# Performance work log

Measured on AMD Instinct MI355X. Metric: run time of the kernel, lower is better.

## Reference

```python
import jax, jax.numpy as jnp
import numpy as np

L, B, H, R = 128, 4, 768, 97
LN_EPS = 1e-5


def setup_inputs() -> dict:
    key = jax.random.key(0)
    ks = jax.random.split(key, 8)
    s = 0.02
    return {
        "h_re1": jax.random.normal(ks[0], (L, B, H), jnp.float32),
        "h_re2": jax.random.normal(ks[1], (L, B, H), jnp.float32),
        "mask": jax.random.uniform(ks[2], (L, B), jnp.float32),
        "Wr": jax.random.normal(ks[3], (H, 2 * H), jnp.float32) * s,
        "br": jnp.zeros((H,), jnp.float32),
        "Wh": jax.random.normal(ks[4], (H, 3 * H), jnp.float32) * s,
        "bh": jnp.zeros((H,), jnp.float32),
        "gamma": jnp.ones((H,), jnp.float32),
        "beta": jnp.zeros((H,), jnp.float32),
        "Wo": jax.random.normal(ks[5], (R, H), jnp.float32) * s,
        "bo": jnp.zeros((R,), jnp.float32),
    }


def reference(h_re1, h_re2, mask, Wr, br, Wh, bh, gamma, beta, Wo, bo):
    # h_re1, h_re2: [L, B, H]; mask: [L, B]
    h = h_re2.shape[-1]
    # global context: tanh(Linear(cat(h_re1,h_re2))), max over length -> [B, H]
    g = jnp.tanh(jnp.einsum('lbi,hi->lbh', jnp.concatenate([h_re1, h_re2], axis=-1), Wr) + br)
    g = jnp.max(g, axis=0)  # [B, H]
    # hid2hid(cat(r1, r2, g)) == r1 @ W1.T + r2 @ W2.T + g @ W3.T + b
    # (avoids materializing the [L,L,B,3H] repeat+cat tensor)
    W1, W2, W3 = Wh[:, :h], Wh[:, h:2 * h], Wh[:, 2 * h:]
    a = jnp.einsum('lbi,hi->lbh', h_re2, W1)          # varies over first pair axis
    b2 = jnp.einsum('lbi,hi->lbh', h_re2, W2)         # varies over second pair axis
    gp = jnp.einsum('bi,hi->bh', g, W3) + bh          # constant over pairs
    pre = a[:, None, :, :] + b2[None, :, :, :] + gp   # [L, L, B, H]
    # LayerNorm over last dim (biased variance, as in torch)
    mu = jnp.mean(pre, axis=-1, keepdims=True)
    var = jnp.var(pre, axis=-1, keepdims=True)
    x = (pre - mu) * jax.lax.rsqrt(var + LN_EPS) * gamma + beta
    x = jax.nn.elu(x)  # dropout is identity in eval mode
    out = jax.nn.sigmoid(jnp.einsum('klbh,rh->klbr', x, Wo) + bo)  # [L, L, B, R]
    # pairwise mask: mask_e1 * mask_e2, broadcast over relation dim
    m = mask[:, None, :, None] * mask[None, :, :, None]
    return out * m
```

## Files before the change

kernel.cpp:

```cpp
#include <hip/hip_runtime.h>
#include <hip/hip_bf16.h>
#include <stdint.h>

#define L_ 128
#define B_ 4
#define H_ 768
#define R_ 97
#define LN_EPS 1e-5f

typedef _Float16 f16x8 __attribute__((ext_vector_type(8)));
typedef _Float16 f16x4 __attribute__((ext_vector_type(4)));
typedef _Float16 f16x2 __attribute__((ext_vector_type(2)));
typedef float f32x4 __attribute__((ext_vector_type(4)));

__global__ __launch_bounds__(256) void prep_all(const float* __restrict__ h1,
                                                const float* __restrict__ h2,
                                                const float* __restrict__ Wr,
                                                const float* __restrict__ Wh,
                                                const float* __restrict__ Wo,
                                                const float* __restrict__ gamma,
                                                const float* __restrict__ beta,
                                                _Float16* __restrict__ ccH,
                                                _Float16* __restrict__ Bp,
                                                _Float16* __restrict__ WoP,
                                                _Float16* __restrict__ gbH) {
  int blk = blockIdx.x;
  if (blk < 512) {
    const float2* s1 = (const float2*)(h1 + (size_t)blk * H_);
    const float2* s2 = (const float2*)(h2 + (size_t)blk * H_);
    f16x2* d = (f16x2*)(ccH + (size_t)blk * (2 * H_));
    for (int i = threadIdx.x; i < H_ / 2; i += 256) {
      float2 v = s1[i]; f16x2 o; o[0] = (_Float16)v.x; o[1] = (_Float16)v.y; d[i] = o;
    }
    for (int i = threadIdx.x; i < H_ / 2; i += 256) {
      float2 v = s2[i]; f16x2 o; o[0] = (_Float16)v.x; o[1] = (_Float16)v.y; d[H_ / 2 + i] = o;
    }
    return;
  }
  blk -= 512;
  if (blk < 6912) {
    int f = (blk * 256 + threadIdx.x) * 2;
    int j = f & 7;
    int u = f >> 3;
    int lidx = u & 63; u >>= 6;
    int nt = u % 144;
    int ks = u / 144;
    int k = ks * 32 + (lidx >> 4) * 8 + j;
    int n = nt * 16 + (lidx & 15);
    float v0, v1;
    if (n < 768) {
      v0 = Wr[(size_t)n * 1536 + k];
      v1 = Wr[(size_t)n * 1536 + k + 1];
    } else if (n < 1536) {
      int n2 = n - 768;
      if (k >= 768) { v0 = Wh[(size_t)n2 * 2304 + (k - 768)]; v1 = Wh[(size_t)n2 * 2304 + (k - 767)]; }
      else { v0 = 0.f; v1 = 0.f; }
    } else {
      int n2 = n - 1536;
      if (k >= 768) { v0 = Wh[(size_t)n2 * 2304 + 768 + (k - 768)]; v1 = Wh[(size_t)n2 * 2304 + 768 + (k - 767)]; }
      else { v0 = 0.f; v1 = 0.f; }
    }
    f16x2 o; o[0] = (_Float16)v0; o[1] = (_Float16)v1;
    *(f16x2*)(Bp + f) = o;
    return;
  }
  blk -= 6912;
  if (blk < 192) {
    int f = (blk * 256 + threadIdx.x) * 2;
    int j = f & 7;
    int u = f >> 3;
    int lidx = u & 63; u >>= 6;
    int nt = u & 7;
    int ks = u >> 3;
    int k = ks * 32 + (lidx >> 4) * 8 + j;
    int n = nt * 16 + (lidx & 15);
    float v0 = 0.f, v1 = 0.f;
    if (n < R_) { v0 = Wo[(size_t)n * H_ + k]; v1 = Wo[(size_t)n * H_ + k + 1]; }
    f16x2 o; o[0] = (_Float16)v0; o[1] = (_Float16)v1;
    *(f16x2*)(WoP + f) = o;
    return;
  }
  blk -= 192;
  int i = blk * 256 + threadIdx.x;
  if (i < H_) {
    gbH[i] = (_Float16)gamma[i];
    gbH[H_ + i] = (_Float16)beta[i];
  }
}

__global__ __launch_bounds__(256) void gemm_big(const _Float16* __restrict__ A,
                                                const _Float16* __restrict__ Bp,
                                                const float* __restrict__ br,
                                                unsigned int* __restrict__ gmaxU,
                                                _Float16* __restrict__ aH,
                                                _Float16* __restrict__ bH) {
  int w = threadIdx.x >> 6, l = threadIdx.x & 63;
  int nb = blockIdx.x, mb = blockIdx.y;
  int row0 = mb * 32 + (w & 1) * 16;
  int nt0 = nb * 4 + (w >> 1) * 2;
  const f16x8* ap = (const f16x8*)(A + (size_t)(row0 + (l & 15)) * 1536 + (l >> 4) * 8);
  const f16x8* bp = (const f16x8*)(Bp + ((size_t)nt0 * 64 + l) * 8);
  f32x4 acc0 = {}, acc1 = {};
  f16x8 ac = ap[0], b0c = bp[0], b1c = bp[64];
  for (int ks = 0; ks < 48; ++ks) {
    f16x8 an = {}, b0n = {}, b1n = {};
    if (ks < 47) {
      an = ap[(ks + 1) * 4];
      b0n = bp[(size_t)(ks + 1) * 9216];
      b1n = bp[(size_t)(ks + 1) * 9216 + 64];
    }
    acc0 = __builtin_amdgcn_mfma_f32_16x16x32_f16(ac, b0c, acc0, 0, 0, 0);
    acc1 = __builtin_amdgcn_mfma_f32_16x16x32_f16(ac, b1c, acc1, 0, 0, 0);
    ac = an; b0c = b0n; b1c = b1n;
  }
#pragma unroll
  for (int q = 0; q < 2; ++q) {
    f32x4 acc = q ? acc1 : acc0;
    int col = nb * 64 + (w >> 1) * 32 + q * 16 + (l & 15);
#pragma unroll
    for (int r = 0; r < 4; ++r) {
      int row = row0 + (l >> 4) * 4 + r;
      float v = acc[r];
      if (col < 768) {
        float t = tanhf(v + br[col]) + 1.0f;
        atomicMax(&gmaxU[(row & 3) * H_ + col], __float_as_uint(t));
      } else if (col < 1536) {
        aH[(size_t)row * H_ + (col - 768)] = (_Float16)v;
      } else {
        bH[(size_t)row * H_ + (col - 1536)] = (_Float16)v;
      }
    }
  }
}

__global__ __launch_bounds__(256) void gp_kernel(const float* __restrict__ Wh,
                                                 const unsigned int* __restrict__ gmaxU,
                                                 const float* __restrict__ bh,
                                                 float* __restrict__ gpv) {
  int n = blockIdx.x;
  int w = threadIdx.x >> 6, l = threadIdx.x & 63;
  const float* wr = Wh + (size_t)n * 2304 + 1536;
  const unsigned int* gm = gmaxU + (size_t)w * H_;
  float s = 0.f;
#pragma unroll
  for (int t = 0; t < 12; ++t) {
    int i = l + 64 * t;
    s += wr[i] * (__uint_as_float(gm[i]) - 1.0f);
  }
#pragma unroll
  for (int off = 32; off; off >>= 1) s += __shfl_xor(s, off);
  if (l == 0) gpv[(size_t)w * H_ + n] = s + bh[n];
}

__global__ __launch_bounds__(256) void stats(const _Float16* __restrict__ aH,
                                             const _Float16* __restrict__ bH,
                                             const float* __restrict__ gpv,
                                             _Float16* __restrict__ aH2,
                                             float* __restrict__ S,
                                             float* __restrict__ Q) {
  int r = blockIdx.x * 4 + (threadIdx.x >> 6);
  int l = threadIdx.x & 63;
  float s = 0.f, q = 0.f;
  if (r < 512) {
    int b = r & 3;
    const f16x4* ap = (const f16x4*)(aH + (size_t)r * H_);
    const float4* gp4 = (const float4*)(gpv + (size_t)b * H_);
    f16x4* op = (f16x4*)(aH2 + (size_t)r * H_);
#pragma unroll
    for (int t = 0; t < 3; ++t) {
      int i = t * 64 + l;
      f16x4 av = ap[i];
      float4 g4 = gp4[i];
      f16x4 o;
      o[0] = (_Float16)((float)av[0] + g4.x);
      o[1] = (_Float16)((float)av[1] + g4.y);
      o[2] = (_Float16)((float)av[2] + g4.z);
      o[3] = (_Float16)((float)av[3] + g4.w);
      op[i] = o;
#pragma unroll
      for (int j = 0; j < 4; ++j) { float y = (float)o[j]; s += y; q += y * y; }
    }
  } else {
    const f16x4* bp = (const f16x4*)(bH + (size_t)(r - 512) * H_);
#pragma unroll
    for (int t = 0; t < 3; ++t) {
      f16x4 bv = bp[t * 64 + l];
#pragma unroll
      for (int j = 0; j < 4; ++j) { float y = (float)bv[j]; s += y; q += y * y; }
    }
  }
#pragma unroll
  for (int off = 32; off; off >>= 1) {
    s += __shfl_xor(s, off);
    q += __shfl_xor(q, off);
  }
  if (l == 0) { S[r] = s; Q[r] = q; }
}

__global__ __launch_bounds__(256) void dotab(const _Float16* __restrict__ aH2,
                                             const _Float16* __restrict__ bH,
                                             const float* __restrict__ S,
                                             const float* __restrict__ Q,
                                             float* __restrict__ mu_arr,
                                             float* __restrict__ rs_arr) {
  int w = threadIdx.x >> 6, l = threadIdx.x & 63;
  int ltq = blockIdx.x, kt = blockIdx.y, b = blockIdx.z;
  int lt = ltq * 4 + w;
  const f16x8* ap = (const f16x8*)(aH2 + ((size_t)(kt * 16 + (l & 15)) * 4 + b) * H_ + (l >> 4) * 8);
  const f16x8* bp = (const f16x8*)(bH + ((size_t)(lt * 16 + (l & 15)) * 4 + b) * H_ + (l >> 4) * 8);
  f32x4 acc = {};
  f16x8 a0 = ap[0], b0 = bp[0], a1 = ap[4], b1 = bp[4];
  for (int ks = 0; ks < 24; ++ks) {
    f16x8 a2 = {}, b2 = {};
    if (ks < 22) { a2 = ap[(ks + 2) * 4]; b2 = bp[(ks + 2) * 4]; }
    acc = __builtin_amdgcn_mfma_f32_16x16x32_f16(a0, b0, acc, 0, 0, 0);
    a0 = a1; b0 = b1; a1 = a2; b1 = b2;
  }
#pragma unroll
  for (int r = 0; r < 4; ++r) {
    int k = kt * 16 + (l >> 4) * 4 + r;
    int lg = lt * 16 + (l & 15);
    int arow = k * 4 + b, brow = lg * 4 + b;
    float mu = (S[arow] + S[512 + brow]) * (1.f / H_);
    float q2 = Q[arow] + Q[512 + brow] + 2.f * acc[r];
    float var = fmaxf(q2 * (1.f / H_) - mu * mu, 0.f);
    float rs = rsqrtf(var + LN_EPS);
    size_t idx = (size_t)k * 512 + (size_t)lg * 4 + b;
    mu_arr[idx] = mu;
    rs_arr[idx] = rs;
  }
}

__global__ __launch_bounds__(256) void fused2(const _Float16* __restrict__ aH2,
                                              const _Float16* __restrict__ bH,
                                              const _Float16* __restrict__ gbH,
                                              const _Float16* __restrict__ WoP,
                                              const float* __restrict__ bo,
                                              const float* __restrict__ mask,
                                              const float* __restrict__ mu_arr,
                                              const float* __restrict__ rs_arr,
                                              float* __restrict__ out) {
  __shared__ __align__(16) _Float16 WoLds[2][4096];
  int tid = threadIdx.x, w = tid >> 6, l = tid & 63;
  int m0 = blockIdx.x * 64;
  int myrow = m0 + w * 16 + (l & 15);
  int b = myrow & 3, li = (myrow >> 2) & 127, kk = myrow >> 9;
  const f16x8* ap = (const f16x8*)(aH2 + ((size_t)kk * 4 + b) * H_ + (l >> 4) * 8);
  const f16x8* bp = (const f16x8*)(bH + ((size_t)li * 4 + b) * H_ + (l >> 4) * 8);
  const f16x8* gp8 = (const f16x8*)(gbH + (l >> 4) * 8);
  const f16x8* be8 = (const f16x8*)(gbH + H_ + (l >> 4) * 8);
  float mu = mu_arr[myrow], rs = rs_arr[myrow];

  const uint4* wog = (const uint4*)WoP;
  uint4* lds0 = (uint4*)&WoLds[0][0];
  lds0[tid] = wog[tid];
  lds0[256 + tid] = wog[256 + tid];
  __syncthreads();

  f32x4 acc[8] = {};
  for (int ks = 0; ks < 24; ++ks) {
    int cur = ks & 1;
    uint4 wo0 = {}, wo1 = {};
    if (ks < 23) {
      wo0 = wog[(ks + 1) * 512 + tid];
      wo1 = wog[(ks + 1) * 512 + 256 + tid];
    }
    f16x8 a8 = ap[ks * 4];
    f16x8 b8 = bp[ks * 4];
    f16x8 g8 = gp8[ks * 4];
    f16x8 e8 = be8[ks * 4];
    f16x8 av;
#pragma unroll
    for (int j = 0; j < 8; ++j) {
      float x = (float)a8[j] + (float)b8[j];
      float t = rs * (float)g8[j];
      float y = (x - mu) * t + (float)e8[j];
      float e = __expf(y) - 1.f;
      y = y > 0.f ? y : e;
      av[j] = (_Float16)y;
    }
    __syncthreads();
    if (ks < 23) {
      uint4* d = (uint4*)&WoLds[cur ^ 1][0];
      d[tid] = wo0;
      d[256 + tid] = wo1;
    }
    __syncthreads();
    const f16x8* bvp = (const f16x8*)&WoLds[cur][0];
#pragma unroll
    for (int q = 0; q < 8; ++q) {
      f16x8 bv = bvp[q * 64 + l];
      acc[q] = __builtin_amdgcn_mfma_f32_16x16x32_f16(av, bv, acc[q], 0, 0, 0);
    }
  }
  float mv[4];
#pragma unroll
  for (int r = 0; r < 4; ++r) {
    int row = m0 + w * 16 + (l >> 4) * 4 + r;
    int bb = row & 3, ll = (row >> 2) & 127, kx = row >> 9;
    mv[r] = mask[kx * 4 + bb] * mask[ll * 4 + bb];
  }
#pragma unroll
  for (int q = 0; q < 8; ++q) {
    int col = q * 16 + (l & 15);
    if (col < R_) {
      float bov = bo[col];
#pragma unroll
      for (int r = 0; r < 4; ++r) {
        int row = m0 + w * 16 + (l >> 4) * 4 + r;
        float z = acc[q][r] + bov;
        out[(size_t)row * R_ + col] = mv[r] / (1.f + __expf(-z));
      }
    }
  }
}

extern "C" void kernel_launch(void* const* d_in, const int* in_sizes, int n_in,
                              void* d_out, int out_size, void* d_ws, size_t ws_size,
                              hipStream_t stream) {
  const float* h1    = (const float*)d_in[0];
  const float* h2    = (const float*)d_in[1];
  const float* mask  = (const float*)d_in[2];
  const float* Wr    = (const float*)d_in[3];
  const float* br    = (const float*)d_in[4];
  const float* Wh    = (const float*)d_in[5];
  const float* bh    = (const float*)d_in[6];
  const float* gamma = (const float*)d_in[7];
  const float* beta  = (const float*)d_in[8];
  const float* Wo    = (const float*)d_in[9];
  const float* bo    = (const float*)d_in[10];
  float* out = (float*)d_out;
  char* ws = (char*)d_ws;

  _Float16* ccH = (_Float16*)ws;                    size_t off = 512 * 1536 * 2;
  _Float16* Bp  = (_Float16*)(ws + off);            off += (size_t)1536 * 2304 * 2;
  _Float16* WoP = (_Float16*)(ws + off);            off += 768 * 128 * 2;
  _Float16* gbH = (_Float16*)(ws + off);            off += 4096;
  _Float16* aH  = (_Float16*)(ws + off);            off += 512 * 768 * 2;
  _Float16* bH  = (_Float16*)(ws + off);            off += 512 * 768 * 2;
  _Float16* aH2 = (_Float16*)(ws + off);            off += 512 * 768 * 2;
  unsigned int* gmaxU = (unsigned int*)(ws + off);  off += 3072 * 4;
  float* gpv = (float*)(ws + off);                  off += 3072 * 4;
  float* S   = (float*)(ws + off);                  off += 1024 * 4;
  float* Q   = (float*)(ws + off);                  off += 1024 * 4;
  float* mu_arr = (float*)(ws + off);               off += 65536 * 4;
  float* rs_arr = (float*)(ws + off);               off += 65536 * 4;

  prep_all<<<512 + 6912 + 192 + 3, 256, 0, stream>>>(h1, h2, Wr, Wh, Wo, gamma, beta,
                                                     ccH, Bp, WoP, gbH);
  hipMemsetAsync(gmaxU, 0, 3072 * 4, stream);

  gemm_big<<<dim3(36, 16), 256, 0, stream>>>(ccH, Bp, br, gmaxU, aH, bH);
  gp_kernel<<<768, 256, 0, stream>>>(Wh, gmaxU, bh, gpv);
  stats<<<256, 256, 0, stream>>>(aH, bH, gpv, aH2, S, Q);
  dotab<<<dim3(2, 8, 4), 256, 0, stream>>>(aH2, bH, S, Q, mu_arr, rs_arr);

  fused2<<<1024, 256, 0, stream>>>(aH2, bH, gbH, WoP, bo, mask, mu_arr, rs_arr, out);
}
```

Baseline: 103.3 us.

## Double k-steps per barrier in fused2, skip padded N tile, fold memset into prep

```diff
diff --git a/kernel.cpp b/kernel.cpp
--- a/kernel.cpp
+++ b/kernel.cpp
@@ -23,7 +23,8 @@
                                                 _Float16* __restrict__ ccH,
                                                 _Float16* __restrict__ Bp,
                                                 _Float16* __restrict__ WoP,
-                                                _Float16* __restrict__ gbH) {
+                                                _Float16* __restrict__ gbH,
+                                                unsigned int* __restrict__ gmaxU) {
   int blk = blockIdx.x;
   if (blk < 512) {
     const float2* s1 = (const float2*)(h1 + (size_t)blk * H_);
@@ -81,11 +82,17 @@
     return;
   }
   blk -= 192;
+  if (blk < 3) {
+    int i = blk * 256 + threadIdx.x;
+    if (i < H_) {
+      gbH[i] = (_Float16)gamma[i];
+      gbH[H_ + i] = (_Float16)beta[i];
+    }
+    return;
+  }
+  blk -= 3;
   int i = blk * 256 + threadIdx.x;
-  if (i < H_) {
-    gbH[i] = (_Float16)gamma[i];
-    gbH[H_ + i] = (_Float16)beta[i];
-  }
+  if (i < B_ * H_) gmaxU[i] = 0u;
 }
 
 __global__ __launch_bounds__(256) void gemm_big(const _Float16* __restrict__ A,
@@ -240,7 +247,7 @@
                                               const float* __restrict__ mu_arr,
                                               const float* __restrict__ rs_arr,
                                               float* __restrict__ out) {
-  __shared__ __align__(16) _Float16 WoLds[2][4096];
+  __shared__ __align__(16) uint4 WoLds[2][1024];
   int tid = threadIdx.x, w = tid >> 6, l = tid & 63;
   int m0 = blockIdx.x * 64;
   int myrow = m0 + w * 16 + (l & 15);
@@ -252,46 +259,49 @@
   float mu = mu_arr[myrow], rs = rs_arr[myrow];
 
   const uint4* wog = (const uint4*)WoP;
-  uint4* lds0 = (uint4*)&WoLds[0][0];
-  lds0[tid] = wog[tid];
-  lds0[256 + tid] = wog[256 + tid];
+  uint4 pf[4];
+#pragma unroll
+  for (int i = 0; i < 4; ++i) WoLds[0][tid + 256 * i] = wog[tid + 256 * i];
+#pragma unroll
+  for (int i = 0; i < 4; ++i) pf[i] = wog[1024 + tid + 256 * i];
   __syncthreads();
 
-  f32x4 acc[8] = {};
-  for (int ks = 0; ks < 24; ++ks) {
-    int cur = ks & 1;
-    uint4 wo0 = {}, wo1 = {};
-    if (ks < 23) {
-      wo0 = wog[(ks + 1) * 512 + tid];
-      wo1 = wog[(ks + 1) * 512 + 256 + tid];
-    }
-    f16x8 a8 = ap[ks * 4];
-    f16x8 b8 = bp[ks * 4];
-    f16x8 g8 = gp8[ks * 4];
-    f16x8 e8 = be8[ks * 4];
-    f16x8 av;
-#pragma unroll
-    for (int j = 0; j < 8; ++j) {
-      float x = (float)a8[j] + (float)b8[j];
-      float t = rs * (float)g8[j];
-      float y = (x - mu) * t + (float)e8[j];
-      float e = __expf(y) - 1.f;
-      y = y > 0.f ? y : e;
-      av[j] = (_Float16)y;
+  f32x4 acc[7] = {};
+  for (int c = 0; c < 12; ++c) {
+    int cur = c & 1;
+    if (c < 11) {
+#pragma unroll
+      for (int i = 0; i < 4; ++i) WoLds[cur ^ 1][tid + 256 * i] = pf[i];
+    }
+    if (c < 10) {
+#pragma unroll
+      for (int i = 0; i < 4; ++i) pf[i] = wog[(size_t)(c + 2) * 1024 + tid + 256 * i];
+    }
+#pragma unroll
+    for (int s = 0; s < 2; ++s) {
+      int ks = 2 * c + s;
+      f16x8 a8 = ap[ks * 4];
+      f16x8 b8 = bp[ks * 4];
+      f16x8 g8 = gp8[ks * 4];
+      f16x8 e8 = be8[ks * 4];
+      f16x8 av;
+#pragma unroll
+      for (int j = 0; j < 8; ++j) {
+        float x = (float)a8[j] + (float)b8[j];
+        float t = rs * (float)g8[j];
+        float y = (x - mu) * t + (float)e8[j];
+        float e = __expf(y) - 1.f;
+        y = y > 0.f ? y : e;
+        av[j] = (_Float16)y;
+      }
+      const f16x8* bvp = (const f16x8*)&WoLds[cur][s * 512];
+#pragma unroll
+      for (int q = 0; q < 7; ++q) {
+        f16x8 bv = bvp[q * 64 + l];
+        acc[q] = __builtin_amdgcn_mfma_f32_16x16x32_f16(av, bv, acc[q], 0, 0, 0);
+      }
     }
     __syncthreads();
-    if (ks < 23) {
-      uint4* d = (uint4*)&WoLds[cur ^ 1][0];
-      d[tid] = wo0;
-      d[256 + tid] = wo1;
-    }
-    __syncthreads();
-    const f16x8* bvp = (const f16x8*)&WoLds[cur][0];
-#pragma unroll
-    for (int q = 0; q < 8; ++q) {
-      f16x8 bv = bvp[q * 64 + l];
-      acc[q] = __builtin_amdgcn_mfma_f32_16x16x32_f16(av, bv, acc[q], 0, 0, 0);
-    }
   }
   float mv[4];
 #pragma unroll
@@ -301,7 +311,7 @@
     mv[r] = mask[kx * 4 + bb] * mask[ll * 4 + bb];
   }
 #pragma unroll
-  for (int q = 0; q < 8; ++q) {
+  for (int q = 0; q < 7; ++q) {
     int col = q * 16 + (l & 15);
     if (col < R_) {
       float bov = bo[col];
@@ -346,9 +356,8 @@
   float* mu_arr = (float*)(ws + off);               off += 65536 * 4;
   float* rs_arr = (float*)(ws + off);               off += 65536 * 4;
 
-  prep_all<<<512 + 6912 + 192 + 3, 256, 0, stream>>>(h1, h2, Wr, Wh, Wo, gamma, beta,
-                                                     ccH, Bp, WoP, gbH);
-  hipMemsetAsync(gmaxU, 0, 3072 * 4, stream);
+  prep_all<<<512 + 6912 + 192 + 3 + 12, 256, 0, stream>>>(h1, h2, Wr, Wh, Wo, gamma, beta,
+                                                          ccH, Bp, WoP, gbH, gmaxU);
 
   gemm_big<<<dim3(36, 16), 256, 0, stream>>>(ccH, Bp, br, gmaxU, aH, bH);
   gp_kernel<<<768, 256, 0, stream>>>(Wh, gmaxU, bh, gpv);
```

Result: slower. 134.2 us (+30.0%).
